# Kernel optimization log

Hardware: AMD Instinct MI355X
Metric: run time of the kernel (lower is better)

Reference implementation:

```python
import jax, jax.numpy as jnp
import numpy as np

N = 100000       # nodes
E = 3200000      # edges (avg degree 32)
IN_F = 256
OUT_F = 128


def setup_inputs() -> dict:
    key = jax.random.key(0)
    k1, k2, k3, k4, k5, k6 = jax.random.split(key, 6)
    x = jax.random.normal(k1, (N, IN_F), dtype=jnp.float32)
    adj_row = jax.random.randint(k2, (E,), 0, N, dtype=jnp.int64)
    adj_col = jax.random.randint(k3, (E,), 0, N, dtype=jnp.int64)
    adj_val = jax.random.uniform(k4, (E,), dtype=jnp.float32)
    stdv = 1.0 / np.sqrt(OUT_F)
    weight = jax.random.uniform(k5, (IN_F, OUT_F), dtype=jnp.float32, minval=-stdv, maxval=stdv)
    bias = jax.random.uniform(k6, (OUT_F,), dtype=jnp.float32, minval=-stdv, maxval=stdv)
    return {"x": x, "adj_row": adj_row, "adj_col": adj_col,
            "adj_val": adj_val, "weight": weight, "bias": bias}


def reference(x, adj_row, adj_col, adj_val, weight, bias):
    # dropout with p=0 is identity
    support = x @ weight                                   # [N, OUT_F] dense GEMM
    # spmm(adj, support): gather neighbor rows, scale by edge value, segment-sum into rows
    gathered = adj_val[:, None] * support[adj_col]         # [E, OUT_F]
    out = jax.ops.segment_sum(gathered, adj_row, num_segments=N)  # [N, OUT_F]
    return jax.nn.relu(out + bias)
```

## Files before the change

### kernel.cpp

```cpp
#include <hip/hip_runtime.h>

#define N_NODES 100000
#define IN_F 256
#define OUT_F 128
#define RPB 64
#define RSHIFT 6
#define NB 1563
#define CAPG 2560
#define CHUNK_SC 8192

typedef short bf16x8 __attribute__((ext_vector_type(8)));
typedef float f32x4  __attribute__((ext_vector_type(4)));

static __device__ __forceinline__ unsigned short f2bf(float f) {
    unsigned int u = __float_as_uint(f);
    u = (u + 0x7FFF + ((u >> 16) & 1)) >> 16;
    return (unsigned short)u;
}

__global__ __launch_bounds__(256) void wt_kernel(const float* __restrict__ w,
                                                 unsigned short* __restrict__ wT,
                                                 int* __restrict__ gcur) {
    int n = blockIdx.x;
    int k = threadIdx.x;
    wT[n * IN_F + k] = f2bf(w[(size_t)k * OUT_F + n]);
    if (blockIdx.x < 7) {
        int i = blockIdx.x * 256 + threadIdx.x;
        if (i < NB) gcur[i] = i * CAPG;
    }
}

__global__ __launch_bounds__(256) void gemm_mfma_kernel(const float* __restrict__ x,
                                                        const unsigned short* __restrict__ wT,
                                                        unsigned short* __restrict__ supb) {
    __shared__ unsigned short A_lds[32][72];
    __shared__ unsigned short B_lds[128][72];

    const int tid  = threadIdx.x;
    const int wave = tid >> 6;
    const int lane = tid & 63;
    const int quad = lane >> 4;
    const int l15  = lane & 15;
    const int rt   = wave & 1;
    const int cg   = (wave >> 1) * 4;
    const int row_base = blockIdx.x * 32;

    f32x4 acc[4];
#pragma unroll
    for (int c = 0; c < 4; ++c) acc[c] = (f32x4){0.f, 0.f, 0.f, 0.f};

    const int s_row = tid >> 3;
    const int s_kc  = (tid & 7) * 8;
    const float* xrow = x + (size_t)(row_base + s_row) * IN_F + s_kc;

    const int b_n  = tid >> 1;
    const int b_kc = (tid & 1) * 32;
    const unsigned short* wrow = wT + (size_t)b_n * IN_F + b_kc;

    for (int k0 = 0; k0 < IN_F; k0 += 64) {
        __syncthreads();

        float4 xa = *(const float4*)(xrow + k0);
        float4 xb = *(const float4*)(xrow + k0 + 4);
        ushort4 ua = {f2bf(xa.x), f2bf(xa.y), f2bf(xa.z), f2bf(xa.w)};
        ushort4 ub = {f2bf(xb.x), f2bf(xb.y), f2bf(xb.z), f2bf(xb.w)};
        *(ushort4*)&A_lds[s_row][s_kc]     = ua;
        *(ushort4*)&A_lds[s_row][s_kc + 4] = ub;

#pragma unroll
        for (int j = 0; j < 4; ++j) {
            float4 wv = *(const float4*)(wrow + k0 + j * 8);
            *(float4*)&B_lds[b_n][b_kc + j * 8] = wv;
        }

        __syncthreads();

#pragma unroll
        for (int ks = 0; ks < 64; ks += 32) {
            bf16x8 af = *(const bf16x8*)&A_lds[rt * 16 + l15][ks + quad * 8];
#pragma unroll
            for (int c = 0; c < 4; ++c) {
                bf16x8 bfr = *(const bf16x8*)&B_lds[(cg + c) * 16 + l15][ks + quad * 8];
                acc[c] = __builtin_amdgcn_mfma_f32_16x16x32_bf16(af, bfr, acc[c], 0, 0, 0);
            }
        }
    }

#pragma unroll
    for (int c = 0; c < 4; ++c) {
#pragma unroll
        for (int r = 0; r < 4; ++r) {
            int orow = row_base + rt * 16 + quad * 4 + r;
            supb[(size_t)orow * OUT_F + (cg + c) * 16 + l15] = f2bf(acc[c][r]);
        }
    }
}

__global__ __launch_bounds__(256) void scatter_kernel(const int* __restrict__ adj_row,
                                                      const int* __restrict__ adj_col,
                                                      const float* __restrict__ adj_val,
                                                      int* __restrict__ gcur,
                                                      int2* __restrict__ ebuf, int E) {
    __shared__ int lh[NB];
    const int tid = threadIdx.x;
    for (int b = tid; b < NB; b += 256) lh[b] = 0;
    const int base = blockIdx.x * CHUNK_SC;
    const int m = min(CHUNK_SC, E - base);
    __syncthreads();

#pragma unroll
    for (int j = 0; j < CHUNK_SC / 256; ++j) {
        int i = j * 256 + tid;
        if (i < m) atomicAdd(&lh[adj_row[base + i] >> RSHIFT], 1);
    }
    __syncthreads();

    for (int b = tid; b < NB; b += 256) {
        int c = lh[b];
        if (c) lh[b] = atomicAdd(&gcur[b], c);
    }
    __syncthreads();

#pragma unroll
    for (int j = 0; j < CHUNK_SC / 256; ++j) {
        int i = j * 256 + tid;
        if (i < m) {
            int r  = adj_row[base + i];
            int bk = r >> RSHIFT;
            int pos = atomicAdd(&lh[bk], 1);
            if (pos < (bk + 1) * CAPG) {
                int2 rec;
                rec.x = adj_col[base + i] | ((r & (RPB - 1)) << 17);
                rec.y = __float_as_int(adj_val[base + i]);
                ebuf[pos] = rec;
            }
        }
    }
}

__global__ __launch_bounds__(512) void spmm_kernel(const int2* __restrict__ ebuf,
                                                   const int* __restrict__ gcur,
                                                   const unsigned short* __restrict__ supb,
                                                   const float* __restrict__ bias,
                                                   float* __restrict__ out) {
    __shared__ int2 se[CAPG];
    __shared__ int cnt[RPB];
    __shared__ int off[RPB];
    __shared__ int cur[RPB];

    const int tid  = threadIdx.x;
    const int b    = blockIdx.x;
    const int wave = tid >> 6;
    const int lane = tid & 63;
    const int f0   = lane * 2;

    const int start = b * CAPG;
    int m = gcur[b] - start;
    if (m > CAPG) m = CAPG;

    if (tid < RPB) cnt[tid] = 0;
    __syncthreads();

    int2 ev[5];
#pragma unroll
    for (int j = 0; j < 5; ++j) {
        int i = j * 512 + tid;
        if (i < m) {
            ev[j] = ebuf[start + i];
            atomicAdd(&cnt[ev[j].x >> 17], 1);
        }
    }
    __syncthreads();

    if (tid < RPB) {
        int v = cnt[tid];
        int s = v;
#pragma unroll
        for (int d = 1; d < RPB; d <<= 1) {
            int t = __shfl_up(s, d, 64);
            if (tid >= d) s += t;
        }
        off[tid] = s - v;
        cur[tid] = s - v;
    }
    __syncthreads();

#pragma unroll
    for (int j = 0; j < 5; ++j) {
        int i = j * 512 + tid;
        if (i < m) {
            int p = atomicAdd(&cur[ev[j].x >> 17], 1);
            se[p] = ev[j];
        }
    }
    __syncthreads();

    float2 acc[8];
#pragma unroll
    for (int j = 0; j < 8; ++j) acc[j] = make_float2(0.f, 0.f);

#pragma unroll
    for (int j = 0; j < 8; ++j) {
        int r = wave * 8 + j;
        int o = off[r];
        int c = cnt[r];
        float2 a = acc[j];
        int i = 0;
        for (; i + 4 <= c; i += 4) {
            int2 e0 = se[o + i + 0];
            int2 e1 = se[o + i + 1];
            int2 e2 = se[o + i + 2];
            int2 e3 = se[o + i + 3];
            unsigned int u0 = *(const unsigned int*)(supb + (size_t)(e0.x & 0x1FFFF) * OUT_F + f0);
            unsigned int u1 = *(const unsigned int*)(supb + (size_t)(e1.x & 0x1FFFF) * OUT_F + f0);
            unsigned int u2 = *(const unsigned int*)(supb + (size_t)(e2.x & 0x1FFFF) * OUT_F + f0);
            unsigned int u3 = *(const unsigned int*)(supb + (size_t)(e3.x & 0x1FFFF) * OUT_F + f0);
            float v0 = __int_as_float(e0.y), v1 = __int_as_float(e1.y);
            float v2 = __int_as_float(e2.y), v3 = __int_as_float(e3.y);
            a.x += v0 * __uint_as_float(u0 << 16);
            a.y += v0 * __uint_as_float(u0 & 0xFFFF0000u);
            a.x += v1 * __uint_as_float(u1 << 16);
            a.y += v1 * __uint_as_float(u1 & 0xFFFF0000u);
            a.x += v2 * __uint_as_float(u2 << 16);
            a.y += v2 * __uint_as_float(u2 & 0xFFFF0000u);
            a.x += v3 * __uint_as_float(u3 << 16);
            a.y += v3 * __uint_as_float(u3 & 0xFFFF0000u);
        }
        for (; i < c; ++i) {
            int2 e = se[o + i];
            unsigned int u = *(const unsigned int*)(supb + (size_t)(e.x & 0x1FFFF) * OUT_F + f0);
            float v = __int_as_float(e.y);
            a.x += v * __uint_as_float(u << 16);
            a.y += v * __uint_as_float(u & 0xFFFF0000u);
        }
        acc[j] = a;
    }

    float2 bv = *((const float2*)bias + lane);
    const int rbase = b << RSHIFT;
#pragma unroll
    for (int j = 0; j < 8; ++j) {
        int grow = rbase + wave * 8 + j;
        if (grow < N_NODES) {
            float2 o;
            o.x = fmaxf(acc[j].x + bv.x, 0.f);
            o.y = fmaxf(acc[j].y + bv.y, 0.f);
            *((float2*)(out + (size_t)grow * OUT_F) + lane) = o;
        }
    }
}

extern "C" void kernel_launch(void* const* d_in, const int* in_sizes, int n_in,
                              void* d_out, int out_size, void* d_ws, size_t ws_size,
                              hipStream_t stream) {
    const float* x       = (const float*)d_in[0];
    const int*   adj_row = (const int*)d_in[1];
    const int*   adj_col = (const int*)d_in[2];
    const float* adj_val = (const float*)d_in[3];
    const float* weight  = (const float*)d_in[4];
    const float* bias    = (const float*)d_in[5];
    float* out = (float*)d_out;
    const int E = in_sizes[1];

    char* p = (char*)d_ws;
    unsigned short* supb = (unsigned short*)p;  p += (size_t)N_NODES * OUT_F * 2;
    int2* ebuf           = (int2*)p;            p += (size_t)NB * CAPG * 8;
    unsigned short* wT   = (unsigned short*)p;  p += (size_t)OUT_F * IN_F * 2;
    int* gcur            = (int*)p;             p += (size_t)NB * 4;

    wt_kernel<<<OUT_F, 256, 0, stream>>>(weight, wT, gcur);
    gemm_mfma_kernel<<<N_NODES / 32, 256, 0, stream>>>(x, wT, supb);
    scatter_kernel<<<(E + CHUNK_SC - 1) / CHUNK_SC, 256, 0, stream>>>(adj_row, adj_col,
                                                                      adj_val, gcur, ebuf, E);
    spmm_kernel<<<NB, 512, 0, stream>>>(ebuf, gcur, supb, bias, out);
}
```

Measured before the change: 402.6 us.

## Stage scatter in LDS sorted by bucket and keep GEMM weights in registers

```diff
diff --git a/kernel.cpp b/kernel.cpp
--- a/kernel.cpp
+++ b/kernel.cpp
@@ -7,7 +7,7 @@
 #define RSHIFT 6
 #define NB 1563
 #define CAPG 2560
-#define CHUNK_SC 8192
+#define CHUNK_SC 4096
 
 typedef short bf16x8 __attribute__((ext_vector_type(8)));
 typedef float f32x4  __attribute__((ext_vector_type(4)));
@@ -33,67 +33,65 @@
 __global__ __launch_bounds__(256) void gemm_mfma_kernel(const float* __restrict__ x,
                                                         const unsigned short* __restrict__ wT,
                                                         unsigned short* __restrict__ supb) {
-    __shared__ unsigned short A_lds[32][72];
-    __shared__ unsigned short B_lds[128][72];
+    __shared__ unsigned short A_lds[32][264];
 
     const int tid  = threadIdx.x;
     const int wave = tid >> 6;
     const int lane = tid & 63;
     const int quad = lane >> 4;
     const int l15  = lane & 15;
-    const int rt   = wave & 1;
-    const int cg   = (wave >> 1) * 4;
     const int row_base = blockIdx.x * 32;
 
-    f32x4 acc[4];
-#pragma unroll
-    for (int c = 0; c < 4; ++c) acc[c] = (f32x4){0.f, 0.f, 0.f, 0.f};
-
-    const int s_row = tid >> 3;
-    const int s_kc  = (tid & 7) * 8;
-    const float* xrow = x + (size_t)(row_base + s_row) * IN_F + s_kc;
-
-    const int b_n  = tid >> 1;
-    const int b_kc = (tid & 1) * 32;
-    const unsigned short* wrow = wT + (size_t)b_n * IN_F + b_kc;
-
-    for (int k0 = 0; k0 < IN_F; k0 += 64) {
-        __syncthreads();
-
-        float4 xa = *(const float4*)(xrow + k0);
-        float4 xb = *(const float4*)(xrow + k0 + 4);
-        ushort4 ua = {f2bf(xa.x), f2bf(xa.y), f2bf(xa.z), f2bf(xa.w)};
-        ushort4 ub = {f2bf(xb.x), f2bf(xb.y), f2bf(xb.z), f2bf(xb.w)};
-        *(ushort4*)&A_lds[s_row][s_kc]     = ua;
-        *(ushort4*)&A_lds[s_row][s_kc + 4] = ub;
-
-#pragma unroll
-        for (int j = 0; j < 4; ++j) {
-            float4 wv = *(const float4*)(wrow + k0 + j * 8);
-            *(float4*)&B_lds[b_n][b_kc + j * 8] = wv;
-        }
-
-        __syncthreads();
-
-#pragma unroll
-        for (int ks = 0; ks < 64; ks += 32) {
-            bf16x8 af = *(const bf16x8*)&A_lds[rt * 16 + l15][ks + quad * 8];
-#pragma unroll
-            for (int c = 0; c < 4; ++c) {
-                bf16x8 bfr = *(const bf16x8*)&B_lds[(cg + c) * 16 + l15][ks + quad * 8];
-                acc[c] = __builtin_amdgcn_mfma_f32_16x16x32_bf16(af, bfr, acc[c], 0, 0, 0);
+    bf16x8 bfrag[2][8];
+    {
+        const unsigned short* wb = wT + (size_t)(wave * 32 + l15) * IN_F + quad * 8;
+#pragma unroll
+        for (int ct = 0; ct < 2; ++ct)
+#pragma unroll
+            for (int ks = 0; ks < 8; ++ks)
+                bfrag[ct][ks] = *(const bf16x8*)(wb + ct * 16 * IN_F + ks * 32);
+    }
+
+    {
+        const float* xb = x + (size_t)row_base * IN_F;
+#pragma unroll
+        for (int i = 0; i < 8; ++i) {
+            int fidx = i * 1024 + tid * 4;
+            float4 a = *(const float4*)(xb + fidx);
+            int r = fidx >> 8;
+            int c = fidx & 255;
+            ushort4 u = {f2bf(a.x), f2bf(a.y), f2bf(a.z), f2bf(a.w)};
+            *(ushort4*)&A_lds[r][c] = u;
+        }
+    }
+    __syncthreads();
+
+    f32x4 acc[2][2];
+#pragma unroll
+    for (int rt = 0; rt < 2; ++rt)
+#pragma unroll
+        for (int ct = 0; ct < 2; ++ct) acc[rt][ct] = (f32x4){0.f, 0.f, 0.f, 0.f};
+
+#pragma unroll
+    for (int ks = 0; ks < 8; ++ks) {
+        bf16x8 a0 = *(const bf16x8*)&A_lds[l15][ks * 32 + quad * 8];
+        bf16x8 a1 = *(const bf16x8*)&A_lds[16 + l15][ks * 32 + quad * 8];
+        acc[0][0] = __builtin_amdgcn_mfma_f32_16x16x32_bf16(a0, bfrag[0][ks], acc[0][0], 0, 0, 0);
+        acc[0][1] = __builtin_amdgcn_mfma_f32_16x16x32_bf16(a0, bfrag[1][ks], acc[0][1], 0, 0, 0);
+        acc[1][0] = __builtin_amdgcn_mfma_f32_16x16x32_bf16(a1, bfrag[0][ks], acc[1][0], 0, 0, 0);
+        acc[1][1] = __builtin_amdgcn_mfma_f32_16x16x32_bf16(a1, bfrag[1][ks], acc[1][1], 0, 0, 0);
+    }
+
+#pragma unroll
+    for (int rt = 0; rt < 2; ++rt)
+#pragma unroll
+        for (int ct = 0; ct < 2; ++ct)
+#pragma unroll
+            for (int r = 0; r < 4; ++r) {
+                int orow = row_base + rt * 16 + quad * 4 + r;
+                int ocol = wave * 32 + ct * 16 + l15;
+                supb[(size_t)orow * OUT_F + ocol] = f2bf(acc[rt][ct][r]);
             }
-        }
-    }
-
-#pragma unroll
-    for (int c = 0; c < 4; ++c) {
-#pragma unroll
-        for (int r = 0; r < 4; ++r) {
-            int orow = row_base + rt * 16 + quad * 4 + r;
-            supb[(size_t)orow * OUT_F + (cg + c) * 16 + l15] = f2bf(acc[c][r]);
-        }
-    }
 }
 
 __global__ __launch_bounds__(256) void scatter_kernel(const int* __restrict__ adj_row,
@@ -101,40 +99,97 @@
                                                       const float* __restrict__ adj_val,
                                                       int* __restrict__ gcur,
                                                       int2* __restrict__ ebuf, int E) {
-    __shared__ int lh[NB];
-    const int tid = threadIdx.x;
-    for (int b = tid; b < NB; b += 256) lh[b] = 0;
+    __shared__ int pref[NB + 1];
+    __shared__ int shf[NB];
+    __shared__ int2 se[CHUNK_SC];
+    __shared__ int wsum[4];
+
+    const int tid  = threadIdx.x;
     const int base = blockIdx.x * CHUNK_SC;
-    const int m = min(CHUNK_SC, E - base);
-    __syncthreads();
-
-#pragma unroll
-    for (int j = 0; j < CHUNK_SC / 256; ++j) {
-        int i = j * 256 + tid;
-        if (i < m) atomicAdd(&lh[adj_row[base + i] >> RSHIFT], 1);
+    const int m    = min(CHUNK_SC, E - base);
+    const int nv   = m >> 2;
+
+    for (int b = tid; b <= NB; b += 256) pref[b] = 0;
+    __syncthreads();
+
+    for (int j = tid; j < nv; j += 256) {
+        int4 r4 = ((const int4*)(adj_row + base))[j];
+        atomicAdd(&pref[r4.x >> RSHIFT], 1);
+        atomicAdd(&pref[r4.y >> RSHIFT], 1);
+        atomicAdd(&pref[r4.z >> RSHIFT], 1);
+        atomicAdd(&pref[r4.w >> RSHIFT], 1);
+    }
+    if (tid < (m & 3)) atomicAdd(&pref[adj_row[base + (nv << 2) + tid] >> RSHIFT], 1);
+    __syncthreads();
+
+    {
+        int loc[7];
+        const int bb = tid * 7;
+        int s = 0;
+#pragma unroll
+        for (int g = 0; g < 7; ++g) {
+            int b = bb + g;
+            int v = (b < NB) ? pref[b] : 0;
+            loc[g] = s;
+            s += v;
+        }
+        const int lane = tid & 63, wv = tid >> 6;
+        int inc = s;
+        for (int d = 1; d < 64; d <<= 1) {
+            int t = __shfl_up(inc, d, 64);
+            if (lane >= d) inc += t;
+        }
+        if (lane == 63) wsum[wv] = inc;
+        __syncthreads();
+        int wb2 = 0;
+        for (int k = 0; k < wv; ++k) wb2 += wsum[k];
+        const int texcl = wb2 + inc - s;
+#pragma unroll
+        for (int g = 0; g < 7; ++g) {
+            int b = bb + g;
+            if (b < NB) pref[b] = texcl + loc[g];
+        }
+        if (tid == 255) pref[NB] = texcl + s;
     }
     __syncthreads();
 
     for (int b = tid; b < NB; b += 256) {
-        int c = lh[b];
-        if (c) lh[b] = atomicAdd(&gcur[b], c);
-    }
-    __syncthreads();
-
-#pragma unroll
-    for (int j = 0; j < CHUNK_SC / 256; ++j) {
-        int i = j * 256 + tid;
-        if (i < m) {
-            int r  = adj_row[base + i];
-            int bk = r >> RSHIFT;
-            int pos = atomicAdd(&lh[bk], 1);
-            if (pos < (bk + 1) * CAPG) {
-                int2 rec;
-                rec.x = adj_col[base + i] | ((r & (RPB - 1)) << 17);
-                rec.y = __float_as_int(adj_val[base + i]);
-                ebuf[pos] = rec;
-            }
-        }
+        int s0 = pref[b];
+        int c  = pref[b + 1] - s0;
+        if (c > 0) shf[b] = atomicAdd(&gcur[b], c) - s0;
+    }
+    __syncthreads();
+
+    for (int j = tid; j < nv; j += 256) {
+        int4   c4 = ((const int4*)(adj_col + base))[j];
+        int4   r4 = ((const int4*)(adj_row + base))[j];
+        float4 v4 = ((const float4*)(adj_val + base))[j];
+        int p;
+        p = atomicAdd(&pref[r4.x >> RSHIFT], 1);
+        se[p] = make_int2(c4.x | ((r4.x & (RPB - 1)) << 17), __float_as_int(v4.x));
+        p = atomicAdd(&pref[r4.y >> RSHIFT], 1);
+        se[p] = make_int2(c4.y | ((r4.y & (RPB - 1)) << 17), __float_as_int(v4.y));
+        p = atomicAdd(&pref[r4.z >> RSHIFT], 1);
+        se[p] = make_int2(c4.z | ((r4.z & (RPB - 1)) << 17), __float_as_int(v4.z));
+        p = atomicAdd(&pref[r4.w >> RSHIFT], 1);
+        se[p] = make_int2(c4.w | ((r4.w & (RPB - 1)) << 17), __float_as_int(v4.w));
+    }
+    if (tid < (m & 3)) {
+        int i = base + (nv << 2) + tid;
+        int r = adj_row[i];
+        int p = atomicAdd(&pref[r >> RSHIFT], 1);
+        se[p] = make_int2(adj_col[i] | ((r & (RPB - 1)) << 17), __float_as_int(adj_val[i]));
+    }
+    __syncthreads();
+
+    for (int p = tid; p < m; p += 256) {
+        int lo = 0, hi = NB - 1;
+        while (lo < hi) {
+            int mid = (lo + hi) >> 1;
+            if (pref[mid] > p) hi = mid; else lo = mid + 1;
+        }
+        int g = shf[lo] + p;
+        if (g < (lo + 1) * CAPG) ebuf[g] = se[p];
     }
 }
 
```

Result: faster. 372.0 us (-7.6%).
